# Kernel optimization log

Measured on AMD Instinct MI355X. Metric: run time of the kernel, lower is better.

The kernel has to match this reference:

```python
import jax, jax.numpy as jnp
import numpy as np

NUM_HEADS = 8
HEAD_DIM = 64
WIN = (8, 8, 8)  # (wT, wH, wW)


def setup_inputs() -> dict:
    key = jax.random.key(0)
    k1, k2, k3 = jax.random.split(key, 3)
    B, T, H, W, C = 2, 16, 32, 32, 512
    d_inner = NUM_HEADS * HEAD_DIM  # 512
    x = jax.random.normal(k1, (B, T * H * W, C), dtype=jnp.float32)
    # torch Linear weights stored transposed as [in, out] for y = x @ w
    w_qkv = jax.random.normal(k2, (C, 3 * d_inner), dtype=jnp.float32) * (C ** -0.5)
    w_proj = jax.random.normal(k3, (d_inner, C), dtype=jnp.float32) * (d_inner ** -0.5)
    b_proj = jnp.zeros((C,), dtype=jnp.float32)
    return {"x": x, "w_qkv": w_qkv, "w_proj": w_proj, "b_proj": b_proj,
            "T": T, "H": H, "W": W}


def reference(x, w_qkv, w_proj, b_proj, T, H, W):
    B, N, C = x.shape
    wT, wH, wW = WIN
    scale = HEAD_DIM ** -0.5
    # module re-derives T if N mismatches T*H*W
    if N != T * H * W:
        T = N // (H * W)
    xv = x.reshape(B, T, H, W, C)
    pt, ph, pw = (-T) % wT, (-H) % wH, (-W) % wW
    if pt or ph or pw:
        xv = jnp.pad(xv, ((0, 0), (0, pt), (0, ph), (0, pw), (0, 0)))
    Tp, Hp, Wp = T + pt, H + ph, W + pw
    nT, nH, nW = Tp // wT, Hp // wH, Wp // wW
    L = wT * wH * wW  # tokens per window
    # window partition: [B*nT*nH*nW, L, C]
    xw = xv.reshape(B, nT, wT, nH, wH, nW, wW, C)
    xw = xw.transpose(0, 1, 3, 5, 2, 4, 6, 7).reshape(-1, L, C)
    # qkv projection (no bias)
    qkv = xw @ w_qkv  # [nw, L, 3*nh*hd]
    q, k, v = jnp.split(qkv, 3, axis=-1)

    def heads(t):
        return t.reshape(t.shape[0], L, NUM_HEADS, HEAD_DIM).transpose(0, 2, 1, 3)

    q, k, v = heads(q), heads(k), heads(v)  # [nw, h, L, d]
    attn = jax.nn.softmax(jnp.einsum('nhid,nhjd->nhij', q, k) * scale, axis=-1)
    o = jnp.einsum('nhij,nhjd->nhid', attn, v)
    o = o.transpose(0, 2, 1, 3).reshape(-1, L, NUM_HEADS * HEAD_DIM)
    o = o @ w_proj + b_proj  # output projection
    # window un-partition
    o = o.reshape(B, nT, nH, nW, wT, wH, wW, C)
    o = o.transpose(0, 1, 4, 2, 5, 3, 6, 7).reshape(B, Tp, Hp, Wp, C)
    return o[:, :T, :H, :W].reshape(B, N, C)
```

## Files before the change

### kernel.cpp

```cpp
#include <hip/hip_runtime.h>
#include <hip/hip_bf16.h>

typedef __hip_bfloat16 bf16;
typedef __attribute__((ext_vector_type(8))) short bf16x8;
typedef __attribute__((ext_vector_type(4))) float f32x4;
typedef __attribute__((ext_vector_type(4))) unsigned int u32x4;

#define MROWS 32768
#define CDIM 512
#define SEL_STRIDE (512*512*64)

__device__ __forceinline__ int win_to_src_row(int m) {
  int win = m >> 9, l = m & 511;
  int b = win >> 5, rr = win & 31;
  int nt = rr >> 4, nh = (rr >> 2) & 3, nw = rr & 3;
  int wt = l >> 6, wh = (l >> 3) & 7, ww = l & 7;
  int tt = nt * 8 + wt, hh = nh * 8 + wh, wp = nw * 8 + ww;
  return (b << 14) + (tt << 10) + (hh << 5) + wp;
}

__device__ __forceinline__ unsigned short bf16bits(bf16 h) {
  return __builtin_bit_cast(unsigned short, h);
}

__device__ __forceinline__ ushort4 pack4(f32x4 a) {
  ushort4 o;
  o.x = bf16bits(__float2bfloat16(a[0]));
  o.y = bf16bits(__float2bfloat16(a[1]));
  o.z = bf16bits(__float2bfloat16(a[2]));
  o.w = bf16bits(__float2bfloat16(a[3]));
  return o;
}

__device__ __forceinline__ unsigned int cvtpk_bf16(float lo, float hi) {
  unsigned int r;
  asm("v_cvt_pk_bf16_f32 %0, %1, %2" : "=v"(r) : "v"(lo), "v"(hi));
  return r;
}

__device__ __forceinline__ int xcd_chunk(int bx, int n) {
  return (bx & 7) * (n >> 3) + (bx >> 3);
}

__global__ __launch_bounds__(256) void transpose_cvt_kernel(
    const float* __restrict__ src, bf16* __restrict__ dst, int R, int C) {
  __shared__ float tile[32][33];
  int bc = blockIdx.x * 32, br = blockIdx.y * 32;
  int tx = threadIdx.x, ty = threadIdx.y;
#pragma unroll
  for (int i = 0; i < 32; i += 8)
    tile[ty + i][tx] = src[(size_t)(br + ty + i) * C + bc + tx];
  __syncthreads();
#pragma unroll
  for (int i = 0; i < 32; i += 8)
    dst[(size_t)(bc + ty + i) * R + br + tx] = __float2bfloat16(tile[tx][ty + i]);
}

__global__ __launch_bounds__(256) void perm_x_kernel(const float* __restrict__ x,
                                                     bf16* __restrict__ xw) {
  const int total = MROWS * (CDIM / 4);
  for (int i = blockIdx.x * 256 + threadIdx.x; i < total; i += 2048 * 256) {
    int m = i >> 7, c4 = (i & 127) * 4;
    int src = win_to_src_row(m);
    float4 v = *(const float4*)(x + (size_t)src * CDIM + c4);
    ushort4 o;
    o.x = bf16bits(__float2bfloat16(v.x));
    o.y = bf16bits(__float2bfloat16(v.y));
    o.z = bf16bits(__float2bfloat16(v.z));
    o.w = bf16bits(__float2bfloat16(v.w));
    *(ushort4*)(xw + (size_t)m * CDIM + c4) = o;
  }
}

#define BM 128
#define BN 128
#define BK 64

__device__ __forceinline__ void gload16(const bf16* g, const bf16* l) {
  __builtin_amdgcn_global_load_lds(
      (const __attribute__((address_space(1))) unsigned int*)g,
      (__attribute__((address_space(3))) unsigned int*)l, 16, 0, 0);
}

template <int MODE, int SWAP>
__global__ __launch_bounds__(256) void gemm_bt_kernel(
    const bf16* __restrict__ A, const bf16* __restrict__ Bt, int Ntiles, int bn0,
    bf16* __restrict__ qkv_out, float* __restrict__ out,
    const float* __restrict__ bias) {
  __shared__ __align__(16) bf16 Asl[BM * BK];
  __shared__ __align__(16) bf16 Bsl[BN * BK];
  const int K = 512;
  int l2 = xcd_chunk(blockIdx.x, gridDim.x);
  int bn = bn0 + (l2 >> 3) % Ntiles;
  int bm = (l2 & 7) + (l2 / (8 * Ntiles)) * 8;
  int t = threadIdx.x, lane = t & 63, w = t >> 6;
  int wr = w >> 1, wc = w & 1;
  int l15 = lane & 15, lh = lane >> 4;
  f32x4 acc[4][4] = {};

  for (int kt = 0; kt < K; kt += BK) {
    __syncthreads();
#pragma unroll
    for (int i = 0; i < 4; ++i) {
      int f = i * 256 + t;
      int row = f >> 3, cb = f & 7;
      gload16(A + (size_t)(bm * BM + row) * K + kt + cb * 8,
              &Asl[(i * 256 + w * 64) * 8]);
    }
#pragma unroll
    for (int i = 0; i < 4; ++i) {
      int f = i * 256 + t;
      int row = f >> 3, cb = f & 7;
      gload16(Bt + (size_t)(bn * BN + row) * K + kt + cb * 8,
              &Bsl[(i * 256 + w * 64) * 8]);
    }
    __syncthreads();
#pragma unroll
    for (int kk = 0; kk < 2; ++kk) {
      bf16x8 af[4], bfr[4];
#pragma unroll
      for (int mi = 0; mi < 4; ++mi)
        af[mi] = *(const bf16x8*)&Asl[(wr * 64 + mi * 16 + l15) * BK + kk * 32 + lh * 8];
#pragma unroll
      for (int nj = 0; nj < 4; ++nj)
        bfr[nj] = *(const bf16x8*)&Bsl[(wc * 64 + nj * 16 + l15) * BK + kk * 32 + lh * 8];
#pragma unroll
      for (int mi = 0; mi < 4; ++mi)
#pragma unroll
        for (int nj = 0; nj < 4; ++nj) {
          if (SWAP)
            acc[mi][nj] = __builtin_amdgcn_mfma_f32_16x16x32_bf16(
                bfr[nj], af[mi], acc[mi][nj], 0, 0, 0);
          else
            acc[mi][nj] = __builtin_amdgcn_mfma_f32_16x16x32_bf16(
                af[mi], bfr[nj], acc[mi][nj], 0, 0, 0);
        }
    }
  }

  if (MODE == 0 && SWAP == 1) {
#pragma unroll
    for (int mi = 0; mi < 4; ++mi) {
      int tok_g = bm * BM + wr * 64 + mi * 16 + l15;
      int win = tok_g >> 9, tk = tok_g & 511;
#pragma unroll
      for (int nj = 0; nj < 4; ++nj) {
        int c = bn * BN + wc * 64 + nj * 16 + lh * 4;
        int sel = c >> 9, cc = c & 511;
        int head = cc >> 6, d0 = cc & 63;
        *(ushort4*)(qkv_out + (size_t)sel * SEL_STRIDE +
                    (((size_t)(win * 8 + head)) * 512 + tk) * 64 + d0) =
            pack4(acc[mi][nj]);
      }
    }
  } else if (MODE == 0) {
#pragma unroll
    for (int mi = 0; mi < 4; ++mi) {
      int tok0 = bm * BM + wr * 64 + mi * 16 + lh * 4;
      int win = tok0 >> 9, tk0 = tok0 & 511;
#pragma unroll
      for (int nj = 0; nj < 4; ++nj) {
        int cc = (bn - 8) * BN + wc * 64 + nj * 16 + l15;
        int head = cc >> 6, d = cc & 63;
        *(ushort4*)(qkv_out + 2 * (size_t)SEL_STRIDE +
                    (((size_t)(win * 8 + head)) * 64 + d) * 512 + tk0) =
            pack4(acc[mi][nj]);
      }
    }
  } else {
#pragma unroll
    for (int mi = 0; mi < 4; ++mi) {
      int row = bm * BM + wr * 64 + mi * 16 + l15;
      int srow = win_to_src_row(row);
      float* op = out + (size_t)srow * CDIM;
#pragma unroll
      for (int nj = 0; nj < 4; ++nj) {
        int col = bn * BN + wc * 64 + nj * 16 + lh * 4;
        float4 bv = *(const float4*)(bias + col);
        float4 v;
        v.x = acc[mi][nj][0] + bv.x;
        v.y = acc[mi][nj][1] + bv.y;
        v.z = acc[mi][nj][2] + bv.z;
        v.w = acc[mi][nj][3] + bv.w;
        *(float4*)(op + col) = v;
      }
    }
  }
}

__global__ __launch_bounds__(256, 2) void attn_kernel(const bf16* __restrict__ qkv_ws,
                                                      bf16* __restrict__ o_ws) {
  int l2 = xcd_chunk(blockIdx.x, 1024);
  int wh = l2 >> 1, qc = l2 & 1;
  int win = wh >> 3, head = wh & 7;
  int t = threadIdx.x, lane = t & 63, w = t >> 6;
  int l15 = lane & 15, lh = lane >> 4;
  const bf16* qb = qkv_ws + (size_t)wh * (512 * 64);
  const bf16* kb = qb + SEL_STRIDE;
  const bf16* vtb = qkv_ws + 2 * (size_t)SEL_STRIDE + (size_t)wh * (64 * 512);

  const float c_scale = 0.18033688011112042f;
  int q0 = qc * 256 + w * 64;
  bf16x8 qf[4][2];
#pragma unroll
  for (int qi = 0; qi < 4; ++qi)
#pragma unroll
    for (int kk = 0; kk < 2; ++kk)
      qf[qi][kk] = *(const bf16x8*)(qb + (size_t)(q0 + qi * 16 + l15) * 64 + kk * 32 + lh * 8);

  int idx0 = (((((2 * lh + 0) & 3) << 4) + l15) << 2);
  int idx1 = (((((2 * lh + 1) & 3) << 4) + l15) << 2);
  int kjsel = lh >> 1;

  f32x4 acco[4][4] = {};
  float lsum[4] = {0.f, 0.f, 0.f, 0.f};
  for (int ck = 0; ck < 16; ++ck) {
    bf16x8 kf[2][2], vf[4];
#pragma unroll
    for (int kj = 0; kj < 2; ++kj) {
      int tok = ck * 32 + kj * 16 + l15;
#pragma unroll
      for (int kk = 0; kk < 2; ++kk)
        kf[kj][kk] = *(const bf16x8*)(kb + (size_t)tok * 64 + kk * 32 + lh * 8);
    }
#pragma unroll
    for (int nj = 0; nj < 4; ++nj)
      vf[nj] = *(const bf16x8*)(vtb + (size_t)(nj * 16 + l15) * 512 + ck * 32 + lh * 8);
#pragma unroll
    for (int qi = 0; qi < 4; ++qi) {
      f32x4 s0 = {}, s1 = {};
#pragma unroll
      for (int kk = 0; kk < 2; ++kk) {
        s0 = __builtin_amdgcn_mfma_f32_16x16x32_bf16(kf[0][kk], qf[qi][kk], s0, 0, 0, 0);
        s1 = __builtin_amdgcn_mfma_f32_16x16x32_bf16(kf[1][kk], qf[qi][kk], s1, 0, 0, 0);
      }
      float p00 = __builtin_exp2f(s0[0] * c_scale);
      float p01 = __builtin_exp2f(s0[1] * c_scale);
      float p02 = __builtin_exp2f(s0[2] * c_scale);
      float p03 = __builtin_exp2f(s0[3] * c_scale);
      float p10 = __builtin_exp2f(s1[0] * c_scale);
      float p11 = __builtin_exp2f(s1[1] * c_scale);
      float p12 = __builtin_exp2f(s1[2] * c_scale);
      float p13 = __builtin_exp2f(s1[3] * c_scale);
      lsum[qi] += ((p00 + p01) + (p02 + p03)) + ((p10 + p11) + (p12 + p13));
      unsigned int pk00 = cvtpk_bf16(p00, p01), pk01 = cvtpk_bf16(p02, p03);
      unsigned int pk10 = cvtpk_bf16(p10, p11), pk11 = cvtpk_bf16(p12, p13);
      unsigned int a0 = (unsigned int)__builtin_amdgcn_ds_bpermute(idx0, (int)pk00);
      unsigned int b0 = (unsigned int)__builtin_amdgcn_ds_bpermute(idx0, (int)pk10);
      unsigned int a1 = (unsigned int)__builtin_amdgcn_ds_bpermute(idx0, (int)pk01);
      unsigned int b1 = (unsigned int)__builtin_amdgcn_ds_bpermute(idx0, (int)pk11);
      unsigned int a2 = (unsigned int)__builtin_amdgcn_ds_bpermute(idx1, (int)pk00);
      unsigned int b2 = (unsigned int)__builtin_amdgcn_ds_bpermute(idx1, (int)pk10);
      unsigned int a3 = (unsigned int)__builtin_amdgcn_ds_bpermute(idx1, (int)pk01);
      unsigned int b3 = (unsigned int)__builtin_amdgcn_ds_bpermute(idx1, (int)pk11);
      u32x4 pu;
      pu[0] = kjsel ? b0 : a0;
      pu[1] = kjsel ? b1 : a1;
      pu[2] = kjsel ? b2 : a2;
      pu[3] = kjsel ? b3 : a3;
      bf16x8 pa = __builtin_bit_cast(bf16x8, pu);
#pragma unroll
      for (int nj = 0; nj < 4; ++nj)
        acco[qi][nj] = __builtin_amdgcn_mfma_f32_16x16x32_bf16(pa, vf[nj], acco[qi][nj], 0, 0, 0);
    }
  }
#pragma unroll
  for (int qi = 0; qi < 4; ++qi) {
    float v = lsum[qi];
    v += __shfl_xor(v, 16);
    v += __shfl_xor(v, 32);
    float inv[4];
#pragma unroll
    for (int r = 0; r < 4; ++r) inv[r] = __frcp_rn(__shfl(v, lh * 4 + r));
#pragma unroll
    for (int nj = 0; nj < 4; ++nj)
#pragma unroll
      for (int r = 0; r < 4; ++r) {
        int row = q0 + qi * 16 + lh * 4 + r;
        int d = nj * 16 + l15;
        o_ws[((size_t)win * 512 + row) * 512 + head * 64 + d] =
            __float2bfloat16(acco[qi][nj][r] * inv[r]);
      }
  }
}

extern "C" void kernel_launch(void* const* d_in, const int* in_sizes, int n_in,
                              void* d_out, int out_size, void* d_ws, size_t ws_size,
                              hipStream_t stream) {
  const float* x = (const float*)d_in[0];
  const float* w_qkv = (const float*)d_in[1];
  const float* w_proj = (const float*)d_in[2];
  const float* b_proj = (const float*)d_in[3];
  float* out = (float*)d_out;

  const size_t OFF_QKV = 33554432;
  const size_t OFF_WQ = OFF_QKV + 100663296;
  const size_t OFF_WP = OFF_WQ + 1572864;
  const size_t NEED = OFF_WP + 524288;
  if (ws_size < NEED) return;

  char* ws = (char*)d_ws;
  bf16* xw = (bf16*)ws;
  bf16* qkv = (bf16*)(ws + OFF_QKV);
  bf16* wqkvT = (bf16*)(ws + OFF_WQ);
  bf16* wprojT = (bf16*)(ws + OFF_WP);
  bf16* o_ws = xw;

  transpose_cvt_kernel<<<dim3(1536 / 32, 512 / 32), dim3(32, 8), 0, stream>>>(w_qkv, wqkvT, 512, 1536);
  transpose_cvt_kernel<<<dim3(512 / 32, 512 / 32), dim3(32, 8), 0, stream>>>(w_proj, wprojT, 512, 512);
  perm_x_kernel<<<2048, 256, 0, stream>>>(x, xw);
  gemm_bt_kernel<0, 1><<<256 * 8, 256, 0, stream>>>(xw, wqkvT, 8, 0, qkv, nullptr, nullptr);
  gemm_bt_kernel<0, 0><<<256 * 4, 256, 0, stream>>>(xw, wqkvT, 4, 8, qkv, nullptr, nullptr);
  attn_kernel<<<1024, 256, 0, stream>>>(qkv, o_ws);
  gemm_bt_kernel<1, 1><<<256 * 4, 256, 0, stream>>>(o_ws, wprojT, 4, 0, nullptr, out, b_proj);
}
```

Baseline: 235.5 us.

## Remap V fragment loads to match P register layout, dropping bpermute shuffles

Removes the eight ds_bpermute cross-lane shuffles per query tile that rearranged the softmax probabilities into MFMA A-operand layout. The V^T fragments are instead loaded as two 8-byte pieces per lane, with the K-dimension ordering permuted so it matches the order the P values already sit in registers. This trades LDS-path permute traffic and selects for narrower, less coalesced global/cache loads of V.

```diff
diff --git a/kernel.cpp b/kernel.cpp
--- a/kernel.cpp
+++ b/kernel.cpp
@@ -208,24 +208,27 @@
     for (int kk = 0; kk < 2; ++kk)
       qf[qi][kk] = *(const bf16x8*)(qb + (size_t)(q0 + qi * 16 + l15) * 64 + kk * 32 + lh * 8);
 
-  int idx0 = (((((2 * lh + 0) & 3) << 4) + l15) << 2);
-  int idx1 = (((((2 * lh + 1) & 3) << 4) + l15) << 2);
-  int kjsel = lh >> 1;
+  const bf16* kp = kb + (size_t)l15 * 64 + lh * 8;
+  const bf16* vp = vtb + (size_t)l15 * 512 + 4 * lh;
 
   f32x4 acco[4][4] = {};
   float lsum[4] = {0.f, 0.f, 0.f, 0.f};
   for (int ck = 0; ck < 16; ++ck) {
-    bf16x8 kf[2][2], vf[4];
-#pragma unroll
-    for (int kj = 0; kj < 2; ++kj) {
-      int tok = ck * 32 + kj * 16 + l15;
+    bf16x8 kf[2][2];
+#pragma unroll
+    for (int kj = 0; kj < 2; ++kj)
 #pragma unroll
       for (int kk = 0; kk < 2; ++kk)
-        kf[kj][kk] = *(const bf16x8*)(kb + (size_t)tok * 64 + kk * 32 + lh * 8);
-    }
-#pragma unroll
-    for (int nj = 0; nj < 4; ++nj)
-      vf[nj] = *(const bf16x8*)(vtb + (size_t)(nj * 16 + l15) * 512 + ck * 32 + lh * 8);
+        kf[kj][kk] = *(const bf16x8*)(kp + (size_t)(ck * 32 + kj * 16) * 64 + kk * 32);
+    bf16x8 vf[4];
+#pragma unroll
+    for (int nj = 0; nj < 4; ++nj) {
+      uint2 a = *(const uint2*)(vp + (size_t)nj * (16 * 512) + ck * 32);
+      uint2 b = *(const uint2*)(vp + (size_t)nj * (16 * 512) + ck * 32 + 16);
+      u32x4 vu;
+      vu[0] = a.x; vu[1] = a.y; vu[2] = b.x; vu[3] = b.y;
+      vf[nj] = __builtin_bit_cast(bf16x8, vu);
+    }
 #pragma unroll
     for (int qi = 0; qi < 4; ++qi) {
       f32x4 s0 = {}, s1 = {};
@@ -243,21 +246,11 @@
       float p12 = __builtin_exp2f(s1[2] * c_scale);
       float p13 = __builtin_exp2f(s1[3] * c_scale);
       lsum[qi] += ((p00 + p01) + (p02 + p03)) + ((p10 + p11) + (p12 + p13));
-      unsigned int pk00 = cvtpk_bf16(p00, p01), pk01 = cvtpk_bf16(p02, p03);
-      unsigned int pk10 = cvtpk_bf16(p10, p11), pk11 = cvtpk_bf16(p12, p13);
-      unsigned int a0 = (unsigned int)__builtin_amdgcn_ds_bpermute(idx0, (int)pk00);
-      unsigned int b0 = (unsigned int)__builtin_amdgcn_ds_bpermute(idx0, (int)pk10);
-      unsigned int a1 = (unsigned int)__builtin_amdgcn_ds_bpermute(idx0, (int)pk01);
-      unsigned int b1 = (unsigned int)__builtin_amdgcn_ds_bpermute(idx0, (int)pk11);
-      unsigned int a2 = (unsigned int)__builtin_amdgcn_ds_bpermute(idx1, (int)pk00);
-      unsigned int b2 = (unsigned int)__builtin_amdgcn_ds_bpermute(idx1, (int)pk10);
-      unsigned int a3 = (unsigned int)__builtin_amdgcn_ds_bpermute(idx1, (int)pk01);
-      unsigned int b3 = (unsigned int)__builtin_amdgcn_ds_bpermute(idx1, (int)pk11);
       u32x4 pu;
-      pu[0] = kjsel ? b0 : a0;
-      pu[1] = kjsel ? b1 : a1;
-      pu[2] = kjsel ? b2 : a2;
-      pu[3] = kjsel ? b3 : a3;
+      pu[0] = cvtpk_bf16(p00, p01);
+      pu[1] = cvtpk_bf16(p02, p03);
+      pu[2] = cvtpk_bf16(p10, p11);
+      pu[3] = cvtpk_bf16(p12, p13);
       bf16x8 pa = __builtin_bit_cast(bf16x8, pu);
 #pragma unroll
       for (int nj = 0; nj < 4; ++nj)
```

Measured after the change: 259.6 us. 10.2% more time.
